# Kernel tuning notes

Measured on AMD Instinct MI355X. Metric: run time of the kernel, lower is better.

Reference implementation:

```python
import jax, jax.numpy as jnp
import numpy as np

H = 1024


def _linear(x, W, b):
    # torch nn.Linear: y = x @ W.T + b
    return jnp.einsum('...i,oi->...o', x, W) + b


def setup_inputs() -> dict:
    key = jax.random.key(0)
    ks = jax.random.split(key, 10)
    s = 1.0 / np.sqrt(H)
    inp = {
        'p': jax.random.normal(ks[0], (8, 4096, H), dtype=jnp.float32),
        'x': jax.random.normal(ks[1], (8, 64, H), dtype=jnp.float32),
        'Wq': jax.random.uniform(ks[2], (H, H), jnp.float32, -s, s),
        'bq': jax.random.uniform(ks[3], (H,), jnp.float32, -s, s),
        'Wk': jax.random.uniform(ks[4], (H, H), jnp.float32, -s, s),
        'bk': jax.random.uniform(ks[5], (H,), jnp.float32, -s, s),
        'Wv': jax.random.uniform(ks[6], (H, H), jnp.float32, -s, s),
        'bv': jax.random.uniform(ks[7], (H,), jnp.float32, -s, s),
        'Wg': jax.random.uniform(ks[8], (1, 2 * H), jnp.float32, -s, s),
        'bg': jax.random.uniform(ks[9], (1,), jnp.float32, -s, s),
    }
    return inp


def reference(p, x, Wq, bq, Wk, bk, Wv, bv, Wg, bg):
    q = _linear(p, Wq, bq)            # (B, S, H)
    k = _linear(x, Wk, bk)            # (B, L, H)
    v = _linear(x, Wv, bv)            # (B, L, H)
    # NOTE: scale applied AFTER softmax, faithful to the original module
    scores = jax.nn.softmax(jnp.einsum('bsh,blh->bsl', q, k), axis=-1)
    scores = scores / jnp.sqrt(jnp.asarray(H, p.dtype))
    out = jnp.einsum('bsl,blh->bsh', scores, v) + p
    g = jax.nn.sigmoid(_linear(jnp.concatenate([out, p], axis=2), Wg, bg))  # (B,S,1)
    return g * out + (1.0 - g) * p
```

## Files before the change

kernel.cpp:

```cpp
#include <hip/hip_runtime.h>

#define H 1024
#define SEQ 4096

typedef float f32x4 __attribute__((ext_vector_type(4)));
typedef short s16x8 __attribute__((ext_vector_type(8)));
typedef unsigned short u16;
typedef u16 u16x4 __attribute__((ext_vector_type(4)));
typedef u16 u16x8 __attribute__((ext_vector_type(8)));

__device__ inline u16 f2bf(float f) {
  union { float f; unsigned u; } v; v.f = f;
  unsigned r = v.u + 0x7fffu + ((v.u >> 16) & 1u);
  return (u16)(r >> 16);
}
__device__ inline float bf2f(u16 b) {
  union { unsigned u; float f; } v; v.u = ((unsigned)b) << 16; return v.f;
}

__device__ __forceinline__ void cvt16(const float* __restrict__ src, u16* __restrict__ dst, int i) {
  const float4* s = reinterpret_cast<const float4*>(src) + (size_t)i * 4;
  float4 a = s[0], b = s[1], c = s[2], d = s[3];
  u16x8 lo, hi;
  lo[0]=f2bf(a.x); lo[1]=f2bf(a.y); lo[2]=f2bf(a.z); lo[3]=f2bf(a.w);
  lo[4]=f2bf(b.x); lo[5]=f2bf(b.y); lo[6]=f2bf(b.z); lo[7]=f2bf(b.w);
  hi[0]=f2bf(c.x); hi[1]=f2bf(c.y); hi[2]=f2bf(c.z); hi[3]=f2bf(c.w);
  hi[4]=f2bf(d.x); hi[5]=f2bf(d.y); hi[6]=f2bf(d.z); hi[7]=f2bf(d.w);
  u16x8* o = reinterpret_cast<u16x8*>(dst) + (size_t)i * 2;
  o[0] = lo; o[1] = hi;
}

__global__ __launch_bounds__(256) void prep_kernel(
    const float* __restrict__ Wq, const float* __restrict__ Wk,
    const float* __restrict__ Wv, const float* __restrict__ x,
    const float* __restrict__ Wg,
    u16* __restrict__ wqTb, u16* __restrict__ wkb, u16* __restrict__ wvb,
    u16* __restrict__ xb, float* __restrict__ wgs, float* __restrict__ zeros) {
  __shared__ u16 tls[64][65];
  int blk = blockIdx.x, t = threadIdx.x;
  if (blk < 256) {
    int ti = blk >> 4, tj = blk & 15;
    int lr = t >> 2, cq = (t & 3) * 16;
    const float* s = Wq + (size_t)(ti * 64 + lr) * H + tj * 64 + cq;
#pragma unroll
    for (int q = 0; q < 4; ++q) {
      float4 v = *reinterpret_cast<const float4*>(s + q * 4);
      tls[lr][cq + q * 4 + 0] = f2bf(v.x);
      tls[lr][cq + q * 4 + 1] = f2bf(v.y);
      tls[lr][cq + q * 4 + 2] = f2bf(v.z);
      tls[lr][cq + q * 4 + 3] = f2bf(v.w);
    }
    __syncthreads();
    u16x8 a, b2;
#pragma unroll
    for (int i = 0; i < 8; ++i) a[i] = tls[cq + i][lr];
#pragma unroll
    for (int i = 0; i < 8; ++i) b2[i] = tls[cq + 8 + i][lr];
    u16* d = wqTb + (size_t)(tj * 64 + lr) * H + ti * 64 + cq;
    *reinterpret_cast<u16x8*>(d) = a;
    *reinterpret_cast<u16x8*>(d + 8) = b2;
  } else if (blk < 512) {
    cvt16(Wk, wkb, (blk - 256) * 256 + t);
  } else if (blk < 768) {
    cvt16(Wv, wvb, (blk - 512) * 256 + t);
  } else if (blk < 896) {
    cvt16(x, xb, (blk - 768) * 256 + t);
  } else {
    int i = t * 4;
    float4 a = *reinterpret_cast<const float4*>(Wg + i);
    float4 b2 = *reinterpret_cast<const float4*>(Wg + H + i);
    float4 o; o.x=a.x+b2.x; o.y=a.y+b2.y; o.z=a.z+b2.z; o.w=a.w+b2.w;
    *reinterpret_cast<float4*>(wgs + i) = o;
    float4 z; z.x=0.f; z.y=0.f; z.z=0.f; z.w=0.f;
    *reinterpret_cast<float4*>(zeros + i) = z;
  }
}

__device__ __forceinline__ void gemm_body(const u16* __restrict__ A, const u16* __restrict__ W,
                                          const float* __restrict__ bias, u16* __restrict__ out,
                                          int mt, int nt, int omode, u16* sm) {
  int m0 = mt * 128, n0 = nt * 128;
  int t = threadIdx.x;
  int wave = t >> 6, lane = t & 63;
  int lane15 = lane & 15, lhi = lane >> 4;
  int wr = wave >> 1, wc = wave & 1;
  u16* a_sm = sm;
  u16* b_sm = sm + 8192;

  f32x4 acc[4][4];
#pragma unroll
  for (int mi = 0; mi < 4; ++mi)
#pragma unroll
    for (int ni = 0; ni < 4; ++ni) acc[mi][ni] = (f32x4)0.f;

  int rsel = wave * 32 + (lane >> 3);
  int csel = (lane & 7) * 8;
  const u16* Ab = A + (size_t)m0 * H + csel;
  const u16* Wb = W + (size_t)n0 * H + csel;

  for (int kt = 0; kt < 16; ++kt) {
    int kc = kt * 64;
#pragma unroll
    for (int j = 0; j < 4; ++j) {
      const u16* ga = Ab + (size_t)(rsel + j * 8) * H + kc;
      const u16* gb = Wb + (size_t)(rsel + j * 8) * H + kc;
      __builtin_amdgcn_global_load_lds((const __attribute__((address_space(1))) unsigned int*)ga,
                                       (__attribute__((address_space(3))) unsigned int*)&a_sm[wave * 2048 + j * 512],
                                       16, 0, 0);
      __builtin_amdgcn_global_load_lds((const __attribute__((address_space(1))) unsigned int*)gb,
                                       (__attribute__((address_space(3))) unsigned int*)&b_sm[wave * 2048 + j * 512],
                                       16, 0, 0);
    }
    __syncthreads();
#pragma unroll
    for (int ks = 0; ks < 2; ++ks) {
      s16x8 af[4], bfr[4];
#pragma unroll
      for (int mi = 0; mi < 4; ++mi)
        af[mi] = *reinterpret_cast<const s16x8*>(&a_sm[(wr * 64 + mi * 16 + lane15) * 64 + ks * 32 + lhi * 8]);
#pragma unroll
      for (int ni = 0; ni < 4; ++ni)
        bfr[ni] = *reinterpret_cast<const s16x8*>(&b_sm[(wc * 64 + ni * 16 + lane15) * 64 + ks * 32 + lhi * 8]);
#pragma unroll
      for (int mi = 0; mi < 4; ++mi)
#pragma unroll
        for (int ni = 0; ni < 4; ++ni)
          acc[mi][ni] = __builtin_amdgcn_mfma_f32_16x16x32_bf16(af[mi], bfr[ni], acc[mi][ni], 0, 0, 0);
    }
    __syncthreads();
  }

  float bqv[4];
#pragma unroll
  for (int ni = 0; ni < 4; ++ni) bqv[ni] = bias[n0 + wc * 64 + ni * 16 + lane15];

  if (omode == 0) {
#pragma unroll
    for (int mi = 0; mi < 4; ++mi)
#pragma unroll
      for (int ni = 0; ni < 4; ++ni)
#pragma unroll
        for (int r = 0; r < 4; ++r)
          sm[(wr * 64 + mi * 16 + lhi * 4 + r) * 128 + wc * 64 + ni * 16 + lane15] =
              f2bf(acc[mi][ni][r] + bqv[ni]);
    __syncthreads();
#pragma unroll
    for (int i = 0; i < 4; ++i) {
      int lin2 = i * 4096 + t * 16;
      int row = lin2 >> 7, col = lin2 & 127;
      u16x8 v0 = *reinterpret_cast<const u16x8*>(&sm[lin2]);
      u16x8 v1 = *reinterpret_cast<const u16x8*>(&sm[lin2 + 8]);
      u16* o = out + (size_t)(m0 + row) * H + n0 + col;
      *reinterpret_cast<u16x8*>(o) = v0;
      *reinterpret_cast<u16x8*>(o + 8) = v1;
    }
  } else {
#pragma unroll
    for (int mi = 0; mi < 4; ++mi)
#pragma unroll
      for (int ni = 0; ni < 4; ++ni) {
        int col = n0 + wc * 64 + ni * 16 + lane15;
#pragma unroll
        for (int r = 0; r < 4; ++r) {
          int row = m0 + wr * 64 + mi * 16 + lhi * 4 + r;
          out[((size_t)(row >> 6) * H + col) * 64 + (row & 63)] = f2bf(acc[mi][ni][r] + bqv[ni]);
        }
      }
  }
}

__global__ __launch_bounds__(256) void kv1_kernel(const u16* __restrict__ xb,
                                                  const u16* __restrict__ wkb, const u16* __restrict__ wvb,
                                                  const float* __restrict__ bk, const float* __restrict__ bv,
                                                  u16* __restrict__ kbf, u16* __restrict__ vTb) {
  __shared__ __align__(16) u16 sm[128 * 128];
  int sel = blockIdx.x >> 5;
  int bid = blockIdx.x & 31;
  if (sel == 0)
    gemm_body(xb, wkb, bk, kbf, bid >> 3, bid & 7, 0, sm);
  else
    gemm_body(xb, wvb, bv, vTb, bid >> 3, bid & 7, 2, sm);
}

__global__ __launch_bounds__(256) void kv2_kernel(const u16* __restrict__ kbf,
                                                  const u16* __restrict__ wqTb,
                                                  const float* __restrict__ zeros,
                                                  u16* __restrict__ ktb,
                                                  const u16* __restrict__ vTb,
                                                  const float* __restrict__ Wg,
                                                  const float* __restrict__ bq,
                                                  float* __restrict__ vg, float* __restrict__ bqk) {
  if (blockIdx.x < 32) {
    __shared__ __align__(16) u16 sm[128 * 128];
    gemm_body(kbf, wqTb, zeros, ktb, blockIdx.x >> 3, blockIdx.x & 7, 0, sm);
  } else {
    __shared__ float bq_s[H];
    __shared__ float partial[4][64];
    int b = blockIdx.x - 32, t = threadIdx.x;
    *reinterpret_cast<float4*>(&bq_s[t * 4]) = *reinterpret_cast<const float4*>(bq + t * 4);
    int l = t & 63, part = t >> 6;
    float s = 0.f;
    const u16* vtp = vTb + ((size_t)b * H + part * 256) * 64 + l;
    for (int h = 0; h < 256; ++h) s += bf2f(vtp[h * 64]) * Wg[part * 256 + h];
    partial[part][l] = s;
    __syncthreads();
    if (t < 64) vg[b * 64 + t] = partial[0][t] + partial[1][t] + partial[2][t] + partial[3][t];
    int row = t >> 2, qp = t & 3;
    const u16* kr = kbf + ((size_t)b * 64 + row) * H + qp * 256;
    float sb = 0.f;
    for (int j = 0; j < 256; j += 8) {
      u16x8 v8 = *reinterpret_cast<const u16x8*>(kr + j);
      const float* bqp = &bq_s[qp * 256 + j];
#pragma unroll
      for (int i2 = 0; i2 < 8; ++i2) sb += bf2f(v8[i2]) * bqp[i2];
    }
    sb += __shfl_xor(sb, 1);
    sb += __shfl_xor(sb, 2);
    if (qp == 0) bqk[b * 64 + row] = sb;
  }
}

__global__ __launch_bounds__(256, 4) void attn_kernel(
    const float* __restrict__ p, const u16* __restrict__ ktb,
    const u16* __restrict__ vT, const float* __restrict__ wgs,
    const float* __restrict__ vg, const float* __restrict__ bqk,
    const float* __restrict__ bg, float* __restrict__ out) {
  int t = threadIdx.x;
  int orig = blockIdx.x;
  int lin = (orig & 7) * 128 + (orig >> 3);
  int b = lin >> 7, st = lin & 127;
  size_t gm0 = (size_t)b * SEQ + (size_t)st * 32;
  int wave = t >> 6, lane = t & 63, lane15 = lane & 15, lhi = lane >> 4;
  int wr = wave & 1, wc2 = wave >> 1;

  __shared__ __align__(16) u16 smem_u[16384];
  __shared__ float wgs_l[H];
  __shared__ float sum_l[2][32], gv_l[2][32];
  __shared__ float gs_l[32], pg_l[32], vg_l[64], bq_l[64];

#define KBUF(bb) (&smem_u[(bb) * 4096])
#define PBUF(bb) (&smem_u[12288 + (bb) * 2048])

  *reinterpret_cast<float4*>(&wgs_l[t * 4]) = *reinterpret_cast<const float4*>(wgs + t * 4);
  if (t < 64) { vg_l[t] = vg[b * 64 + t]; bq_l[t] = bqk[b * 64 + t]; }

  const u16* kb = ktb + (size_t)b * 64 * H;
  int ar = t >> 3, aq = t & 7;
  int awz = (ar & 7) << 3;
  const float* prow = p + (gm0 + ar) * H + aq * 8;
  float pgs = 0.f;

#define KSTAGE(buf, kc)                                                                   \
  {                                                                                       \
    _Pragma("unroll")                                                                     \
    for (int j = 0; j < 2; ++j) {                                                         \
      int row_ = j * 32 + wave * 8 + (lane >> 3);                                         \
      int off_ = (kc) + (((lane & 7) * 8) ^ ((row_ & 7) << 3));                           \
      __builtin_amdgcn_global_load_lds(                                                   \
          (const __attribute__((address_space(1))) unsigned int*)(kb + (size_t)row_ * H + off_), \
          (__attribute__((address_space(3))) unsigned int*)(KBUF(buf) + j * 2048 + wave * 512),  \
          16, 0, 0);                                                                      \
    }                                                                                     \
  }

#define CVT_WRITE(buf, R, kc)                                                             \
  {                                                                                       \
    const float* w_ = &wgs_l[(kc) + aq * 8];                                              \
    pgs += R[0].x*w_[0]+R[0].y*w_[1]+R[0].z*w_[2]+R[0].w*w_[3]                            \
         + R[1].x*w_[4]+R[1].y*w_[5]+R[1].z*w_[6]+R[1].w*w_[7];                           \
    u16x8 o_;                                                                             \
    o_[0]=f2bf(R[0].x); o_[1]=f2bf(R[0].y); o_[2]=f2bf(R[0].z); o_[3]=f2bf(R[0].w);       \
    o_[4]=f2bf(R[1].x); o_[5]=f2bf(R[1].y); o_[6]=f2bf(R[1].z); o_[7]=f2bf(R[1].w);       \
    *reinterpret_cast<u16x8*>(&PBUF(buf)[ar * 64 + ((aq * 8) ^ awz)]) = o_;               \
  }

#define PLOAD(R, kc)                                                                      \
  {                                                                                       \
    const float* pr_ = prow + (kc);                                                       \
    R[0] = *reinterpret_cast<const float4*>(pr_);                                         \
    R[1] = *reinterpret_cast<const float4*>(pr_ + 4);                                     \
  }

  float4 rA[2], rB[2], rC[2];
  KSTAGE(0, 0);
  KSTAGE(1, 64);
  PLOAD(rA, 0);
  PLOAD(rB, 64);
  PLOAD(rC, 128);
  __syncthreads();
  CVT_WRITE(0, rA, 0);
  PLOAD(rA, 192);
  asm volatile("s_waitcnt lgkmcnt(0)" ::: "memory");
  __builtin_amdgcn_s_barrier();
  asm volatile("" ::: "memory");

  f32x4 sacc[2];
  sacc[0] = (f32x4)0.f;
  sacc[1] = (f32x4)0.f;
  int aswz = (lane15 & 7) << 3;

  for (int kt = 0; kt < 16; ++kt) {
    int cur3 = kt % 3, cur2 = kt & 1;
    if (kt < 14) KSTAGE((kt + 2) % 3, (kt + 2) * 64);
    __builtin_amdgcn_sched_barrier(0);
    if (kt < 15) {
      int sel = (kt + 1) % 3;
      if (sel == 0)      { CVT_WRITE(cur2 ^ 1, rA, (kt + 1) * 64); if (kt < 12) PLOAD(rA, (kt + 4) * 64); }
      else if (sel == 1) { CVT_WRITE(cur2 ^ 1, rB, (kt + 1) * 64); if (kt < 12) PLOAD(rB, (kt + 4) * 64); }
      else               { CVT_WRITE(cur2 ^ 1, rC, (kt + 1) * 64); if (kt < 12) PLOAD(rC, (kt + 4) * 64); }
    }
#pragma unroll
    for (int ks2 = 0; ks2 < 2; ++ks2) {
      int col = ks2 * 32 + lhi * 8;
      s16x8 ap = *reinterpret_cast<const s16x8*>(&PBUF(cur2)[(wr * 16 + lane15) * 64 + (col ^ aswz)]);
#pragma unroll
      for (int ni = 0; ni < 2; ++ni) {
        int brow = wc2 * 32 + ni * 16 + lane15;
        s16x8 bk8 = *reinterpret_cast<const s16x8*>(&KBUF(cur3)[brow * 64 + (col ^ ((brow & 7) << 3))]);
        sacc[ni] = __builtin_amdgcn_mfma_f32_16x16x32_bf16(ap, bk8, sacc[ni], 0, 0, 0);
      }
    }
    if (kt <= 11) {
      asm volatile("s_waitcnt vmcnt(6) lgkmcnt(0)" ::: "memory");
    } else if (kt == 12) {
      asm volatile("s_waitcnt vmcnt(4) lgkmcnt(0)" ::: "memory");
    } else if (kt == 13) {
      asm volatile("s_waitcnt vmcnt(2) lgkmcnt(0)" ::: "memory");
    } else {
      asm volatile("s_waitcnt vmcnt(0) lgkmcnt(0)" ::: "memory");
    }
    __builtin_amdgcn_s_barrier();
    asm volatile("" ::: "memory");
  }

  pgs += __shfl_xor(pgs, 1);
  pgs += __shfl_xor(pgs, 2);
  pgs += __shfl_xor(pgs, 4);
  if (aq == 0) pg_l[ar] = pgs;

  u16* P_lds = PBUF(0);
  {
    float vgl[2], bql[2];
#pragma unroll
    for (int ni = 0; ni < 2; ++ni) {
      int c = wc2 * 32 + ni * 16 + lane15;
      vgl[ni] = vg_l[c];
      bql[ni] = bq_l[c];
    }
#pragma unroll
    for (int r = 0; r < 4; ++r) {
      int row = wr * 16 + lhi * 4 + r;
      float e0 = __expf(sacc[0][r] + bql[0]);
      float e1 = __expf(sacc[1][r] + bql[1]);
      float se = e0 + e1;
      float sv = e0 * vgl[0] + e1 * vgl[1];
      se += __shfl_xor(se, 1); se += __shfl_xor(se, 2);
      se += __shfl_xor(se, 4); se += __shfl_xor(se, 8);
      sv += __shfl_xor(sv, 1); sv += __shfl_xor(sv, 2);
      sv += __shfl_xor(sv, 4); sv += __shfl_xor(sv, 8);
      P_lds[row * 72 + wc2 * 32 + lane15] = f2bf(e0);
      P_lds[row * 72 + wc2 * 32 + 16 + lane15] = f2bf(e1);
      if (lane15 == 0) { sum_l[wc2][row] = se; gv_l[wc2][row] = sv; }
    }
  }
  __syncthreads();

  if (t < 32) {
    float ssum = sum_l[0][t] + sum_l[1][t];
    float inv = 1.f / (32.f * ssum);
    float logit = (gv_l[0][t] + gv_l[1][t]) * inv + pg_l[t] + bg[0];
    gs_l[t] = inv / (1.f + __expf(-logit));
  }

  s16x8 pa[2][2];
#pragma unroll
  for (int mi = 0; mi < 2; ++mi)
#pragma unroll
    for (int ks = 0; ks < 2; ++ks)
      pa[mi][ks] = *reinterpret_cast<const s16x8*>(&P_lds[(mi * 16 + lane15) * 72 + ks * 32 + lhi * 8]);
  asm volatile("s_waitcnt lgkmcnt(0)" ::: "memory");
  __syncthreads();

  {
    const u16* vb = vT + (size_t)b * H * 64;
    float* sc = reinterpret_cast<float*>(&smem_u[0]) + wave * 2048;
#pragma unroll
    for (int hcc = 0; hcc < 4; ++hcc) {
      int hbase = wave * 256 + hcc * 64;
      f32x4 acc[2][4];
#pragma unroll
      for (int mi = 0; mi < 2; ++mi)
#pragma unroll
        for (int ni = 0; ni < 4; ++ni) acc[mi][ni] = (f32x4)0.f;
#pragma unroll
      for (int ks = 0; ks < 2; ++ks) {
        s16x8 bv8[4];
#pragma unroll
        for (int ni = 0; ni < 4; ++ni)
          bv8[ni] = *reinterpret_cast<const s16x8*>(vb + (size_t)(hbase + ni * 16 + lane15) * 64 + ks * 32 + lhi * 8);
#pragma unroll
        for (int mi = 0; mi < 2; ++mi)
#pragma unroll
          for (int ni = 0; ni < 4; ++ni)
            acc[mi][ni] = __builtin_amdgcn_mfma_f32_16x16x32_bf16(pa[mi][ks], bv8[ni], acc[mi][ni], 0, 0, 0);
      }
      int swz = (lhi & 1) << 4;
#pragma unroll
      for (int mi = 0; mi < 2; ++mi)
#pragma unroll
        for (int ni = 0; ni < 4; ++ni)
#pragma unroll
          for (int r = 0; r < 4; ++r)
            sc[(mi * 16 + lhi * 4 + r) * 64 + ((ni * 16 + lane15) ^ swz)] = acc[mi][ni][r];
      asm volatile("s_waitcnt lgkmcnt(0)" ::: "memory");
      __builtin_amdgcn_sched_barrier(0);
#pragma unroll
      for (int ii = 0; ii < 8; ++ii) {
        int flat4 = ii * 64 + lane;
        int lrow = flat4 >> 4;
        int c4 = flat4 & 15;
        int scol = (c4 * 4) ^ (((lrow >> 2) & 1) << 4);
        f32x4 a = *reinterpret_cast<const f32x4*>(&sc[lrow * 64 + scol]);
        size_t grow = gm0 + lrow;
        float f = gs_l[lrow];
        float4 pr4 = *reinterpret_cast<const float4*>(&p[grow * H + hbase + c4 * 4]);
        f32x4 o;
        o[0] = pr4.x + f * a[0];
        o[1] = pr4.y + f * a[1];
        o[2] = pr4.z + f * a[2];
        o[3] = pr4.w + f * a[3];
        *reinterpret_cast<f32x4*>(&out[grow * H + hbase + c4 * 4]) = o;
      }
      asm volatile("s_waitcnt lgkmcnt(0)" ::: "memory");
    }
  }
#undef KSTAGE
#undef CVT_WRITE
#undef PLOAD
#undef KBUF
#undef PBUF
}

extern "C" void kernel_launch(void* const* d_in, const int* in_sizes, int n_in,
                              void* d_out, int out_size, void* d_ws, size_t ws_size,
                              hipStream_t stream) {
  const float* p  = (const float*)d_in[0];
  const float* x  = (const float*)d_in[1];
  const float* Wq = (const float*)d_in[2];
  const float* bq = (const float*)d_in[3];
  const float* Wk = (const float*)d_in[4];
  const float* bk = (const float*)d_in[5];
  const float* Wv = (const float*)d_in[6];
  const float* bv = (const float*)d_in[7];
  const float* Wg = (const float*)d_in[8];
  const float* bg = (const float*)d_in[9];
  float* out = (float*)d_out;

  char* ws = (char*)d_ws;
  u16* wqTb    = (u16*)(ws);
  u16* wkb     = (u16*)(ws + 2097152);
  u16* wvb     = (u16*)(ws + 4194304);
  u16* xb      = (u16*)(ws + 6291456);
  u16* kbf     = (u16*)(ws + 7340032);
  u16* ktb     = (u16*)(ws + 8388608);
  u16* vTb     = (u16*)(ws + 9437184);
  float* wgs   = (float*)(ws + 10485760);
  float* zeros = (float*)(ws + 10489856);
  float* vg    = (float*)(ws + 10493952);
  float* bqk   = (float*)(ws + 10498048);

  prep_kernel<<<897, 256, 0, stream>>>(Wq, Wk, Wv, x, Wg, wqTb, wkb, wvb, xb, wgs, zeros);
  kv1_kernel<<<64, 256, 0, stream>>>(xb, wkb, wvb, bk, bv, kbf, vTb);
  kv2_kernel<<<40, 256, 0, stream>>>(kbf, wqTb, zeros, ktb, vTb, Wg, bq, vg, bqk);
  attn_kernel<<<1024, 256, 0, stream>>>(p, ktb, vTb, wgs, vg, bqk, bg, out);
}
```

Before: 120.3 us.

## Load QK score operands directly into registers, dropping the LDS staging pipeline

The score GEMM used to stage K tiles into LDS with global_load_lds and convert p to bf16 into a double-buffered LDS tile, with a barrier every k-step. Now each lane loads its own p fragment (fp32) and K fragment (bf16) straight from global memory into registers, converts them in registers and feeds the MFMAs, using a two-deep register double buffer and no barriers. This removes LDS traffic and synchronisation from the main loop. In exchange, p is loaded redundantly by the two column-waves, K is loaded by every wave in the block, the global access pattern is less coalesced, and register pressure rises.

```diff
diff --git a/kernel.cpp b/kernel.cpp
--- a/kernel.cpp
+++ b/kernel.cpp
@@ -238,107 +238,69 @@
   __shared__ float sum_l[2][32], gv_l[2][32];
   __shared__ float gs_l[32], pg_l[32], vg_l[64], bq_l[64];
 
-#define KBUF(bb) (&smem_u[(bb) * 4096])
-#define PBUF(bb) (&smem_u[12288 + (bb) * 2048])
-
   *reinterpret_cast<float4*>(&wgs_l[t * 4]) = *reinterpret_cast<const float4*>(wgs + t * 4);
   if (t < 64) { vg_l[t] = vg[b * 64 + t]; bq_l[t] = bqk[b * 64 + t]; }
-
-  const u16* kb = ktb + (size_t)b * 64 * H;
-  int ar = t >> 3, aq = t & 7;
-  int awz = (ar & 7) << 3;
-  const float* prow = p + (gm0 + ar) * H + aq * 8;
-  float pgs = 0.f;
-
-#define KSTAGE(buf, kc)                                                                   \
-  {                                                                                       \
-    _Pragma("unroll")                                                                     \
-    for (int j = 0; j < 2; ++j) {                                                         \
-      int row_ = j * 32 + wave * 8 + (lane >> 3);                                         \
-      int off_ = (kc) + (((lane & 7) * 8) ^ ((row_ & 7) << 3));                           \
-      __builtin_amdgcn_global_load_lds(                                                   \
-          (const __attribute__((address_space(1))) unsigned int*)(kb + (size_t)row_ * H + off_), \
-          (__attribute__((address_space(3))) unsigned int*)(KBUF(buf) + j * 2048 + wave * 512),  \
-          16, 0, 0);                                                                      \
-    }                                                                                     \
-  }
-
-#define CVT_WRITE(buf, R, kc)                                                             \
-  {                                                                                       \
-    const float* w_ = &wgs_l[(kc) + aq * 8];                                              \
-    pgs += R[0].x*w_[0]+R[0].y*w_[1]+R[0].z*w_[2]+R[0].w*w_[3]                            \
-         + R[1].x*w_[4]+R[1].y*w_[5]+R[1].z*w_[6]+R[1].w*w_[7];                           \
-    u16x8 o_;                                                                             \
-    o_[0]=f2bf(R[0].x); o_[1]=f2bf(R[0].y); o_[2]=f2bf(R[0].z); o_[3]=f2bf(R[0].w);       \
-    o_[4]=f2bf(R[1].x); o_[5]=f2bf(R[1].y); o_[6]=f2bf(R[1].z); o_[7]=f2bf(R[1].w);       \
-    *reinterpret_cast<u16x8*>(&PBUF(buf)[ar * 64 + ((aq * 8) ^ awz)]) = o_;               \
-  }
-
-#define PLOAD(R, kc)                                                                      \
-  {                                                                                       \
-    const float* pr_ = prow + (kc);                                                       \
-    R[0] = *reinterpret_cast<const float4*>(pr_);                                         \
-    R[1] = *reinterpret_cast<const float4*>(pr_ + 4);                                     \
-  }
-
-  float4 rA[2], rB[2], rC[2];
-  KSTAGE(0, 0);
-  KSTAGE(1, 64);
-  PLOAD(rA, 0);
-  PLOAD(rB, 64);
-  PLOAD(rC, 128);
   __syncthreads();
-  CVT_WRITE(0, rA, 0);
-  PLOAD(rA, 192);
-  asm volatile("s_waitcnt lgkmcnt(0)" ::: "memory");
-  __builtin_amdgcn_s_barrier();
-  asm volatile("" ::: "memory");
+
+  const float* pbase = p + (gm0 + wr * 16 + lane15) * H + lhi * 8;
+  const u16* kbase = ktb + ((size_t)b * 64 + wc2 * 32 + lane15) * H + lhi * 8;
 
   f32x4 sacc[2];
   sacc[0] = (f32x4)0.f;
   sacc[1] = (f32x4)0.f;
-  int aswz = (lane15 & 7) << 3;
-
-  for (int kt = 0; kt < 16; ++kt) {
-    int cur3 = kt % 3, cur2 = kt & 1;
-    if (kt < 14) KSTAGE((kt + 2) % 3, (kt + 2) * 64);
-    __builtin_amdgcn_sched_barrier(0);
-    if (kt < 15) {
-      int sel = (kt + 1) % 3;
-      if (sel == 0)      { CVT_WRITE(cur2 ^ 1, rA, (kt + 1) * 64); if (kt < 12) PLOAD(rA, (kt + 4) * 64); }
-      else if (sel == 1) { CVT_WRITE(cur2 ^ 1, rB, (kt + 1) * 64); if (kt < 12) PLOAD(rB, (kt + 4) * 64); }
-      else               { CVT_WRITE(cur2 ^ 1, rC, (kt + 1) * 64); if (kt < 12) PLOAD(rC, (kt + 4) * 64); }
-    }
-#pragma unroll
-    for (int ks2 = 0; ks2 < 2; ++ks2) {
-      int col = ks2 * 32 + lhi * 8;
-      s16x8 ap = *reinterpret_cast<const s16x8*>(&PBUF(cur2)[(wr * 16 + lane15) * 64 + (col ^ aswz)]);
-#pragma unroll
-      for (int ni = 0; ni < 2; ++ni) {
-        int brow = wc2 * 32 + ni * 16 + lane15;
-        s16x8 bk8 = *reinterpret_cast<const s16x8*>(&KBUF(cur3)[brow * 64 + (col ^ ((brow & 7) << 3))]);
-        sacc[ni] = __builtin_amdgcn_mfma_f32_16x16x32_bf16(ap, bk8, sacc[ni], 0, 0, 0);
-      }
-    }
-    if (kt <= 11) {
-      asm volatile("s_waitcnt vmcnt(6) lgkmcnt(0)" ::: "memory");
-    } else if (kt == 12) {
-      asm volatile("s_waitcnt vmcnt(4) lgkmcnt(0)" ::: "memory");
-    } else if (kt == 13) {
-      asm volatile("s_waitcnt vmcnt(2) lgkmcnt(0)" ::: "memory");
-    } else {
-      asm volatile("s_waitcnt vmcnt(0) lgkmcnt(0)" ::: "memory");
-    }
-    __builtin_amdgcn_s_barrier();
-    asm volatile("" ::: "memory");
-  }
-
-  pgs += __shfl_xor(pgs, 1);
-  pgs += __shfl_xor(pgs, 2);
-  pgs += __shfl_xor(pgs, 4);
-  if (aq == 0) pg_l[ar] = pgs;
-
-  u16* P_lds = PBUF(0);
+  float pgs = 0.f;
+
+#define LOADX(PF, KF, kc)                                                   \
+  {                                                                         \
+    PF[0] = *reinterpret_cast<const f32x4*>(pbase + (kc));                  \
+    PF[1] = *reinterpret_cast<const f32x4*>(pbase + (kc) + 4);              \
+    PF[2] = *reinterpret_cast<const f32x4*>(pbase + (kc) + 32);             \
+    PF[3] = *reinterpret_cast<const f32x4*>(pbase + (kc) + 36);             \
+    KF[0] = *reinterpret_cast<const s16x8*>(kbase + (kc));                  \
+    KF[1] = *reinterpret_cast<const s16x8*>(kbase + 16 * H + (kc));         \
+    KF[2] = *reinterpret_cast<const s16x8*>(kbase + (kc) + 32);             \
+    KF[3] = *reinterpret_cast<const s16x8*>(kbase + 16 * H + (kc) + 32);    \
+  }
+
+#define COMPX(PF, KF, kc)                                                   \
+  {                                                                         \
+    const float* w_ = &wgs_l[(kc) + lhi * 8];                               \
+    pgs += PF[0][0]*w_[0] + PF[0][1]*w_[1] + PF[0][2]*w_[2] + PF[0][3]*w_[3]  \
+         + PF[1][0]*w_[4] + PF[1][1]*w_[5] + PF[1][2]*w_[6] + PF[1][3]*w_[7]  \
+         + PF[2][0]*w_[32] + PF[2][1]*w_[33] + PF[2][2]*w_[34] + PF[2][3]*w_[35] \
+         + PF[3][0]*w_[36] + PF[3][1]*w_[37] + PF[3][2]*w_[38] + PF[3][3]*w_[39]; \
+    s16x8 a0_, a1_;                                                         \
+    a0_[0]=f2bf(PF[0][0]); a0_[1]=f2bf(PF[0][1]); a0_[2]=f2bf(PF[0][2]); a0_[3]=f2bf(PF[0][3]); \
+    a0_[4]=f2bf(PF[1][0]); a0_[5]=f2bf(PF[1][1]); a0_[6]=f2bf(PF[1][2]); a0_[7]=f2bf(PF[1][3]); \
+    a1_[0]=f2bf(PF[2][0]); a1_[1]=f2bf(PF[2][1]); a1_[2]=f2bf(PF[2][2]); a1_[3]=f2bf(PF[2][3]); \
+    a1_[4]=f2bf(PF[3][0]); a1_[5]=f2bf(PF[3][1]); a1_[6]=f2bf(PF[3][2]); a1_[7]=f2bf(PF[3][3]); \
+    sacc[0] = __builtin_amdgcn_mfma_f32_16x16x32_bf16(a0_, KF[0], sacc[0], 0, 0, 0); \
+    sacc[1] = __builtin_amdgcn_mfma_f32_16x16x32_bf16(a0_, KF[1], sacc[1], 0, 0, 0); \
+    sacc[0] = __builtin_amdgcn_mfma_f32_16x16x32_bf16(a1_, KF[2], sacc[0], 0, 0, 0); \
+    sacc[1] = __builtin_amdgcn_mfma_f32_16x16x32_bf16(a1_, KF[3], sacc[1], 0, 0, 0); \
+  }
+
+  {
+    f32x4 pfA[4], pfB[4];
+    s16x8 kfA[4], kfB[4];
+    LOADX(pfA, kfA, 0);
+    LOADX(pfB, kfB, 64);
+#pragma unroll
+    for (int kt2 = 0; kt2 < 7; ++kt2) {
+      COMPX(pfA, kfA, kt2 * 128);
+      LOADX(pfA, kfA, kt2 * 128 + 128);
+      COMPX(pfB, kfB, kt2 * 128 + 64);
+      LOADX(pfB, kfB, kt2 * 128 + 192);
+    }
+    COMPX(pfA, kfA, 896);
+    COMPX(pfB, kfB, 960);
+  }
+
+  pgs += __shfl_xor(pgs, 16);
+  pgs += __shfl_xor(pgs, 32);
+  if (wc2 == 0 && lane < 16) pg_l[wr * 16 + lane15] = pgs;
+
+  u16* P_lds = &smem_u[12288];
   {
     float vgl[2], bql[2];
 #pragma unroll
@@ -434,11 +396,8 @@
       asm volatile("s_waitcnt lgkmcnt(0)" ::: "memory");
     }
   }
-#undef KSTAGE
-#undef CVT_WRITE
-#undef PLOAD
-#undef KBUF
-#undef PBUF
+#undef LOADX
+#undef COMPX
 }
 
 extern "C" void kernel_launch(void* const* d_in, const int* in_sizes, int n_in,
```

Measured after the change: 244.7 us. 2.03x slower.
